# Optimization experiments

Hardware: AMD Instinct MI355X
Metric: run time of the kernel (lower is better)

The kernel has to match this reference:

```python
import jax, jax.numpy as jnp
import numpy as np

B, T, C, HS = 8, 2048, 1024, 64


def setup_inputs() -> dict:
    key = jax.random.key(0)
    kx, kq, kk, kv = jax.random.split(key, 4)
    x = jax.random.normal(kx, (B, T, C), dtype=jnp.float32)
    # torch Linear(C, HS, bias=False): weight [HS, C], y = x @ W.T -> store as [C, HS]
    Wq = jax.random.normal(kq, (C, HS), dtype=jnp.float32) * (C ** -0.5)
    Wk = jax.random.normal(kk, (C, HS), dtype=jnp.float32) * (C ** -0.5)
    Wv = jax.random.normal(kv, (C, HS), dtype=jnp.float32) * (C ** -0.5)
    return {"x": x, "Wq": Wq, "Wk": Wk, "Wv": Wv}


def reference(x, Wq, Wk, Wv):
    _, t, c = x.shape
    q = jnp.einsum('btc,ch->bth', x, Wq)
    k = jnp.einsum('btc,ch->bth', x, Wk)
    v = jnp.einsum('btc,ch->bth', x, Wv)
    # NOTE: original scales by C**-0.5 (hidden_dim), not head_size**-0.5
    scores = jnp.einsum('bth,bsh->bts', q, k) * (c ** -0.5)  # [B,T,T]
    causal = jnp.tril(jnp.ones((t, t), dtype=bool))
    scores = jnp.where(causal, scores, -jnp.inf)
    probs = jax.nn.softmax(scores, axis=-1)  # dropout p=0.0 -> identity
    out = jnp.einsum('bts,bsh->bth', probs, v)  # [B,T,HS]
    return out
```

## Files before the change

### kernel.cpp

```cpp
#include <hip/hip_runtime.h>
#include <hip/hip_bf16.h>

#define B_ 8
#define T_ 2048
#define C_ 1024
#define HS_ 64

typedef float f32x4 __attribute__((ext_vector_type(4)));
typedef __bf16 bf16x8 __attribute__((ext_vector_type(8)));
typedef __bf16 bf16x4 __attribute__((ext_vector_type(4)));

__device__ __forceinline__ void gld_lds16(const void* g, void* l) {
    __builtin_amdgcn_global_load_lds(
        (const __attribute__((address_space(1))) void*)g,
        (__attribute__((address_space(3))) void*)l, 16, 0, 0);
}


__global__ __launch_bounds__(256) void wt_kernel(const float* __restrict__ Wq,
                                                 const float* __restrict__ Wk,
                                                 const float* __restrict__ Wv,
                                                 __bf16* __restrict__ wt) {
    __shared__ float tile[64][65];
    int mb = blockIdx.x >> 4;
    int k0 = (blockIdx.x & 15) * 64;
    const float* W = (mb == 0) ? Wq : (mb == 1 ? Wk : Wv);
    int c = threadIdx.x & 63;
#pragma unroll
    for (int r = threadIdx.x >> 6; r < 64; r += 4)
        tile[r][c] = W[(size_t)(k0 + r) * 64 + c];
    __syncthreads();
    float scale = (mb == 0) ? 0.03125f : 1.0f;
    int kk = threadIdx.x & 63;
#pragma unroll
    for (int n = threadIdx.x >> 6; n < 64; n += 4) {
        int col = (((kk >> 3) ^ (n & 7)) * 8) + (kk & 7);
        wt[(size_t)(mb * 64 + n) * C_ + k0 + col] = (__bf16)(tile[kk][n] * scale);
    }
}

__global__ __launch_bounds__(512) void qkv_kernel(const float* __restrict__ x,
                                                  const __bf16* __restrict__ wt,
                                                  __bf16* __restrict__ qf,
                                                  __bf16* __restrict__ kf,
                                                  __bf16* __restrict__ vf) {
    __shared__ __align__(16) char smem[57344];
    __bf16* xs0 = (__bf16*)smem;
    __bf16* xs1 = (__bf16*)(smem + 4096);
    __bf16* ws0 = (__bf16*)(smem + 8192);
    __bf16* ws1 = (__bf16*)(smem + 32768);

    const int tid = threadIdx.x;
    const int w = tid >> 6, lane = tid & 63, lq = lane & 15, lg = lane >> 4;
    const int m0 = blockIdx.x * 32;
    const int mt = w & 1;
    const int ntb = (w >> 1) * 3;

    f32x4 acc[3];
#pragma unroll
    for (int i = 0; i < 3; ++i) acc[i] = (f32x4)0.0f;

    const int xrow = tid >> 3, xch = tid & 7;
    float4 xr0, xr1;
    const int wslot0 = w * 3 * 64 + lane;

    if (tid < 256) {
        const float* xp = x + (size_t)(m0 + xrow) * C_ + xch * 8;
        xr0 = *(const float4*)xp;
        xr1 = *(const float4*)(xp + 4);
    }
#pragma unroll
    for (int s = 0; s < 3; ++s) {
        int slot = wslot0 + s * 64;
        gld_lds16(wt + (size_t)(slot >> 3) * C_ + (slot & 7) * 8,
                  ws0 + (w * 3 + s) * 512);
    }
    if (tid < 256) {
        bf16x8 xb;
#pragma unroll
        for (int j = 0; j < 4; ++j) { xb[j] = (__bf16)xr0[j]; xb[4 + j] = (__bf16)xr1[j]; }
        *(bf16x8*)(xs0 + xrow * 64 + ((xch ^ (xrow & 7)) * 8)) = xb;
    }

    for (int kt = 0; kt < 16; ++kt) {
        __syncthreads();
        __bf16* xsc = (kt & 1) ? xs1 : xs0;
        __bf16* wsc = (kt & 1) ? ws1 : ws0;
        __bf16* xsn = (kt & 1) ? xs0 : xs1;
        __bf16* wsn = (kt & 1) ? ws0 : ws1;
        if (kt < 15) {
            int k0 = (kt + 1) * 64;
            if (tid < 256) {
                const float* xp = x + (size_t)(m0 + xrow) * C_ + k0 + xch * 8;
                xr0 = *(const float4*)xp;
                xr1 = *(const float4*)(xp + 4);
            }
#pragma unroll
            for (int s = 0; s < 3; ++s) {
                int slot = wslot0 + s * 64;
                gld_lds16(wt + (size_t)(slot >> 3) * C_ + k0 + (slot & 7) * 8,
                          wsn + (w * 3 + s) * 512);
            }
        }
#pragma unroll
        for (int ks = 0; ks < 2; ++ks) {
            int r = mt * 16 + lq;
            bf16x8 a = *(const bf16x8*)(xsc + r * 64 + (((ks * 4 + lg) ^ (r & 7)) * 8));
#pragma unroll
            for (int i = 0; i < 3; ++i) {
                int rw = (ntb + i) * 16 + lq;
                bf16x8 b = *(const bf16x8*)(wsc + rw * 64 + (((ks * 4 + lg) ^ (rw & 7)) * 8));
                acc[i] = __builtin_amdgcn_mfma_f32_16x16x32_bf16(a, b, acc[i], 0, 0, 0);
            }
        }
        if (kt < 15 && tid < 256) {
            bf16x8 xb;
#pragma unroll
            for (int j = 0; j < 4; ++j) { xb[j] = (__bf16)xr0[j]; xb[4 + j] = (__bf16)xr1[j]; }
            *(bf16x8*)(xsn + xrow * 64 + ((xch ^ (xrow & 7)) * 8)) = xb;
        }
    }
    __syncthreads();

    __bf16(*obuf)[208] = (__bf16(*)[208])smem;
#pragma unroll
    for (int i = 0; i < 3; ++i)
#pragma unroll
        for (int r = 0; r < 4; ++r)
            obuf[mt * 16 + lg * 4 + r][(ntb + i) * 16 + lq] = (__bf16)acc[i][r];
    __syncthreads();

    if (w < 4) {
        int mg = w & 1, half = w >> 1;
        size_t qt16 = (size_t)(m0 >> 4) + mg;
        bf16x8 vq = *(const bf16x8*)&obuf[mg * 16 + lq][half * 32 + lg * 8];
        bf16x8 vk = *(const bf16x8*)&obuf[mg * 16 + lq][64 + half * 32 + lg * 8];
        *(bf16x8*)(qf + ((qt16 * 2 + half) * 64 + lane) * 8) = vq;
        *(bf16x8*)(kf + ((qt16 * 2 + half) * 64 + lane) * 8) = vk;
    } else {
        int ntv = w - 4;
        bf16x8 vv;
#pragma unroll
        for (int j = 0; j < 8; ++j)
            vv[j] = obuf[lg * 8 + j][128 + ntv * 16 + lq];
        size_t kt32 = (size_t)(m0 >> 5);
        *(bf16x8*)(vf + ((kt32 * 4 + ntv) * 64 + lane) * 8) = vv;
    }
}

__global__ __launch_bounds__(512, 4) void attn_kernel(const __bf16* __restrict__ qf,
                                                      const __bf16* __restrict__ kf,
                                                      const __bf16* __restrict__ vf,
                                                      float* __restrict__ out) {
    __shared__ float olds[8][16][64];
    __shared__ float mlds[8][16], llds[8][16];
    __shared__ __align__(16) __bf16 plds[8][16 * 72];

    int w    = threadIdx.x >> 6;
    int lane = threadIdx.x & 63;
    int lq = lane & 15, lg = lane >> 4;

    int b  = blockIdx.x & 7;
    int q0 = (63 - (blockIdx.x >> 3)) * 32;
    int qs = w >> 2;
    int wk = w & 3;
    int qt = q0 + qs * 16;

    size_t qbase = ((size_t)b * 128 + (qt >> 4)) * 2;
    bf16x8 aq0 = *(const bf16x8*)(qf + ((qbase + 0) * 64 + lane) * 8);
    bf16x8 aq1 = *(const bf16x8*)(qf + ((qbase + 1) * 64 + lane) * 8);

    f32x4 o[4];
#pragma unroll
    for (int nt = 0; nt < 4; ++nt) o[nt] = (f32x4)0.0f;
    float m_s = -1e30f, l_s = 0.f;

    __bf16* pw = &plds[w][0];

    int ntiles = (qt + 79) >> 6;
    for (int kt = wk; kt < ntiles; kt += 4) {
        int s0 = kt * 64;
        f32x4 s[4];
        __builtin_amdgcn_s_setprio(1);
#pragma unroll
        for (int ct = 0; ct < 4; ++ct) {
            size_t kbase = ((size_t)b * 128 + (s0 >> 4) + ct) * 2;
            bf16x8 k0 = *(const bf16x8*)(kf + ((kbase + 0) * 64 + lane) * 8);
            bf16x8 k1 = *(const bf16x8*)(kf + ((kbase + 1) * 64 + lane) * 8);
            f32x4 a = (f32x4)0.0f;
            a = __builtin_amdgcn_mfma_f32_16x16x32_bf16(k0, aq0, a, 0, 0, 0);
            a = __builtin_amdgcn_mfma_f32_16x16x32_bf16(k1, aq1, a, 0, 0, 0);
            s[ct] = a;
        }
        __builtin_amdgcn_s_setprio(0);
        if (s0 + 63 > qt) {
#pragma unroll
            for (int ct = 0; ct < 4; ++ct)
#pragma unroll
                for (int r = 0; r < 4; ++r)
                    if (s0 + ct * 16 + lg * 4 + r > qt + lq) s[ct][r] = -1e30f;
        }
        bf16x8 bv[2][4];
#pragma unroll
        for (int ks = 0; ks < 2; ++ks)
#pragma unroll
            for (int nt = 0; nt < 4; ++nt)
                bv[ks][nt] = *(const bf16x8*)(vf +
                    (((size_t)(b * 64 + (s0 >> 5) + ks) * 4 + nt) * 64 + lane) * 8);
        float pm = -1e30f;
#pragma unroll
        for (int ct = 0; ct < 4; ++ct)
#pragma unroll
            for (int r = 0; r < 4; ++r) pm = fmaxf(pm, s[ct][r]);
        pm = fmaxf(pm, __shfl_xor(pm, 16));
        pm = fmaxf(pm, __shfl_xor(pm, 32));
        bool need = __any(pm > m_s);
        float al = 1.0f;
        if (need) {
            float mn = fmaxf(m_s, pm);
            al = __expf(m_s - mn);
            m_s = mn;
        }
        float rs = 0.f;
        f32x4 p[4];
#pragma unroll
        for (int ct = 0; ct < 4; ++ct)
#pragma unroll
            for (int r = 0; r < 4; ++r) {
                p[ct][r] = __expf(s[ct][r] - m_s);
                rs += p[ct][r];
            }
        rs += __shfl_xor(rs, 16);
        rs += __shfl_xor(rs, 32);
        if (need) {
            l_s = l_s * al + rs;
            float alr[4];
#pragma unroll
            for (int r = 0; r < 4; ++r) alr[r] = __shfl(al, lg * 4 + r);
#pragma unroll
            for (int nt = 0; nt < 4; ++nt)
#pragma unroll
                for (int r = 0; r < 4; ++r) o[nt][r] *= alr[r];
        } else {
            l_s += rs;
        }
#pragma unroll
        for (int ct = 0; ct < 4; ++ct) {
            bf16x4 qv;
#pragma unroll
            for (int r = 0; r < 4; ++r) qv[r] = (__bf16)p[ct][r];
            *(bf16x4*)&pw[lq * 72 + ct * 16 + lg * 4] = qv;
        }
        asm volatile("" ::: "memory");
        bf16x8 pa0 = *(const bf16x8*)&pw[lq * 72 + lg * 8];
        bf16x8 pa1 = *(const bf16x8*)&pw[lq * 72 + 32 + lg * 8];
        __builtin_amdgcn_s_setprio(1);
#pragma unroll
        for (int nt = 0; nt < 4; ++nt) {
            o[nt] = __builtin_amdgcn_mfma_f32_16x16x32_bf16(pa0, bv[0][nt], o[nt], 0, 0, 0);
            o[nt] = __builtin_amdgcn_mfma_f32_16x16x32_bf16(pa1, bv[1][nt], o[nt], 0, 0, 0);
        }
        __builtin_amdgcn_s_setprio(0);
    }

    asm volatile("" ::: "memory");
#pragma unroll
    for (int nt = 0; nt < 4; ++nt)
#pragma unroll
        for (int r = 0; r < 4; ++r)
            olds[w][lg * 4 + r][nt * 16 + lq] = o[nt][r];
    if (lg == 0) {
        mlds[w][lq] = m_s;
        llds[w][lq] = l_s;
    }
    __syncthreads();

    int row = threadIdx.x >> 4;
    int c4  = (threadIdx.x & 15) * 4;
    int wb  = (row >> 4) * 4;
    int r16 = row & 15;
    float M = -1e30f;
#pragma unroll
    for (int w2 = 0; w2 < 4; ++w2) M = fmaxf(M, mlds[wb + w2][r16]);
    float L = 0.f;
    f32x4 oa = (f32x4)0.0f;
#pragma unroll
    for (int w2 = 0; w2 < 4; ++w2) {
        float sc = __expf(mlds[wb + w2][r16] - M);
        L += sc * llds[wb + w2][r16];
        const float* op = &olds[wb + w2][r16][c4];
#pragma unroll
        for (int j = 0; j < 4; ++j) oa[j] += sc * op[j];
    }
    float inv = 1.0f / L;
    float4 st;
    st.x = oa[0] * inv; st.y = oa[1] * inv; st.z = oa[2] * inv; st.w = oa[3] * inv;
    *(float4*)(out + ((size_t)b * T_ + q0 + row) * HS_ + c4) = st;
}

extern "C" void kernel_launch(void* const* d_in, const int* in_sizes, int n_in,
                              void* d_out, int out_size, void* d_ws, size_t ws_size,
                              hipStream_t stream) {
    const float* x  = (const float*)d_in[0];
    const float* Wq = (const float*)d_in[1];
    const float* Wk = (const float*)d_in[2];
    const float* Wv = (const float*)d_in[3];
    char* ws = (char*)d_ws;
    __bf16* wt = (__bf16*)ws;
    __bf16* qf = (__bf16*)(ws + 393216);
    __bf16* kf = (__bf16*)(ws + 2490368);
    __bf16* vf = (__bf16*)(ws + 4587520);
    float* out = (float*)d_out;

    wt_kernel<<<dim3(48), dim3(256), 0, stream>>>(Wq, Wk, Wv, wt);
    qkv_kernel<<<dim3(512), dim3(512), 0, stream>>>(x, wt, qf, kf, vf);
    attn_kernel<<<dim3(512), dim3(512), 0, stream>>>(qf, kf, vf, out);
}
```

Baseline: 38.91 us.

## Halve attention key tile to 32 and alias LDS buffers for higher occupancy

Shrinks the per-iteration key tile from 64 to 32 columns, which cuts the score, P and V register footprint. Launch bounds rise to 8 blocks per CU. The P staging buffer and the final O reduction buffer now share one LDS allocation, separated by an extra barrier, to lower LDS per block. The aim is more resident waves to hide global-load latency, at the cost of twice as many loop iterations with more softmax and shuffle overhead per MFMA, and finer causal work balance.

New measurement: 53.84 us. 1.38x slower.

```diff
diff --git a/kernel.cpp b/kernel.cpp
--- a/kernel.cpp
+++ b/kernel.cpp
@@ -148,23 +148,22 @@
     }
 }
 
-__global__ __launch_bounds__(512, 4) void attn_kernel(const __bf16* __restrict__ qf,
+__global__ __launch_bounds__(512, 8) void attn_kernel(const __bf16* __restrict__ qf,
                                                       const __bf16* __restrict__ kf,
                                                       const __bf16* __restrict__ vf,
                                                       float* __restrict__ out) {
-    __shared__ float olds[8][16][64];
-    __shared__ float mlds[8][16], llds[8][16];
-    __shared__ __align__(16) __bf16 plds[8][16 * 72];
-
-    int w    = threadIdx.x >> 6;
-    int lane = threadIdx.x & 63;
-    int lq = lane & 15, lg = lane >> 4;
-
-    int b  = blockIdx.x & 7;
-    int q0 = (63 - (blockIdx.x >> 3)) * 32;
-    int qs = w >> 2;
-    int wk = w & 3;
-    int qt = q0 + qs * 16;
+    __shared__ __align__(16) char smem[33792];
+    float* mlds = (float*)(smem + 32768);
+    float* llds = (float*)(smem + 33280);
+
+    const int tid = threadIdx.x;
+    const int w = tid >> 6, lane = tid & 63, lq = lane & 15, lg = lane >> 4;
+
+    const int b  = blockIdx.x & 7;
+    const int q0 = (63 - (blockIdx.x >> 3)) * 32;
+    const int qs = w >> 2;
+    const int wk = w & 3;
+    const int qt = q0 + qs * 16;
 
     size_t qbase = ((size_t)b * 128 + (qt >> 4)) * 2;
     bf16x8 aq0 = *(const bf16x8*)(qf + ((qbase + 0) * 64 + lane) * 8);
@@ -175,15 +174,15 @@
     for (int nt = 0; nt < 4; ++nt) o[nt] = (f32x4)0.0f;
     float m_s = -1e30f, l_s = 0.f;
 
-    __bf16* pw = &plds[w][0];
-
-    int ntiles = (qt + 79) >> 6;
+    __bf16* pw = (__bf16*)(smem + w * 1280);
+
+    int ntiles = (qt + 47) >> 5;
     for (int kt = wk; kt < ntiles; kt += 4) {
-        int s0 = kt * 64;
-        f32x4 s[4];
+        int s0 = kt * 32;
+        f32x4 s[2];
         __builtin_amdgcn_s_setprio(1);
 #pragma unroll
-        for (int ct = 0; ct < 4; ++ct) {
+        for (int ct = 0; ct < 2; ++ct) {
             size_t kbase = ((size_t)b * 128 + (s0 >> 4) + ct) * 2;
             bf16x8 k0 = *(const bf16x8*)(kf + ((kbase + 0) * 64 + lane) * 8);
             bf16x8 k1 = *(const bf16x8*)(kf + ((kbase + 1) * 64 + lane) * 8);
@@ -193,25 +192,20 @@
             s[ct] = a;
         }
         __builtin_amdgcn_s_setprio(0);
-        if (s0 + 63 > qt) {
-#pragma unroll
-            for (int ct = 0; ct < 4; ++ct)
+        if (s0 + 31 > qt) {
+#pragma unroll
+            for (int ct = 0; ct < 2; ++ct)
 #pragma unroll
                 for (int r = 0; r < 4; ++r)
                     if (s0 + ct * 16 + lg * 4 + r > qt + lq) s[ct][r] = -1e30f;
         }
-        bf16x8 bv[2][4];
-#pragma unroll
-        for (int ks = 0; ks < 2; ++ks)
-#pragma unroll
-            for (int nt = 0; nt < 4; ++nt)
-                bv[ks][nt] = *(const bf16x8*)(vf +
-                    (((size_t)(b * 64 + (s0 >> 5) + ks) * 4 + nt) * 64 + lane) * 8);
-        float pm = -1e30f;
-#pragma unroll
-        for (int ct = 0; ct < 4; ++ct)
-#pragma unroll
-            for (int r = 0; r < 4; ++r) pm = fmaxf(pm, s[ct][r]);
+        bf16x8 bv[4];
+#pragma unroll
+        for (int nt = 0; nt < 4; ++nt)
+            bv[nt] = *(const bf16x8*)(vf +
+                (((size_t)(b * 64 + (s0 >> 5)) * 4 + nt) * 64 + lane) * 8);
+        float pm = fmaxf(fmaxf(fmaxf(s[0][0], s[0][1]), fmaxf(s[0][2], s[0][3])),
+                         fmaxf(fmaxf(s[1][0], s[1][1]), fmaxf(s[1][2], s[1][3])));
         pm = fmaxf(pm, __shfl_xor(pm, 16));
         pm = fmaxf(pm, __shfl_xor(pm, 32));
         bool need = __any(pm > m_s);
@@ -222,13 +216,12 @@
             m_s = mn;
         }
         float rs = 0.f;
-        f32x4 p[4];
-#pragma unroll
-        for (int ct = 0; ct < 4; ++ct)
+#pragma unroll
+        for (int ct = 0; ct < 2; ++ct)
 #pragma unroll
             for (int r = 0; r < 4; ++r) {
-                p[ct][r] = __expf(s[ct][r] - m_s);
-                rs += p[ct][r];
+                s[ct][r] = __expf(s[ct][r] - m_s);
+                rs += s[ct][r];
             }
         rs += __shfl_xor(rs, 16);
         rs += __shfl_xor(rs, 32);
@@ -245,50 +238,48 @@
             l_s += rs;
         }
 #pragma unroll
-        for (int ct = 0; ct < 4; ++ct) {
+        for (int ct = 0; ct < 2; ++ct) {
             bf16x4 qv;
 #pragma unroll
-            for (int r = 0; r < 4; ++r) qv[r] = (__bf16)p[ct][r];
-            *(bf16x4*)&pw[lq * 72 + ct * 16 + lg * 4] = qv;
+            for (int r = 0; r < 4; ++r) qv[r] = (__bf16)s[ct][r];
+            *(bf16x4*)&pw[lq * 40 + ct * 16 + lg * 4] = qv;
         }
         asm volatile("" ::: "memory");
-        bf16x8 pa0 = *(const bf16x8*)&pw[lq * 72 + lg * 8];
-        bf16x8 pa1 = *(const bf16x8*)&pw[lq * 72 + 32 + lg * 8];
+        bf16x8 pa = *(const bf16x8*)&pw[lq * 40 + lg * 8];
         __builtin_amdgcn_s_setprio(1);
 #pragma unroll
-        for (int nt = 0; nt < 4; ++nt) {
-            o[nt] = __builtin_amdgcn_mfma_f32_16x16x32_bf16(pa0, bv[0][nt], o[nt], 0, 0, 0);
-            o[nt] = __builtin_amdgcn_mfma_f32_16x16x32_bf16(pa1, bv[1][nt], o[nt], 0, 0, 0);
-        }
+        for (int nt = 0; nt < 4; ++nt)
+            o[nt] = __builtin_amdgcn_mfma_f32_16x16x32_bf16(pa, bv[nt], o[nt], 0, 0, 0);
         __builtin_amdgcn_s_setprio(0);
     }
 
-    asm volatile("" ::: "memory");
+    __syncthreads();
+    float* olds = (float*)smem;
 #pragma unroll
     for (int nt = 0; nt < 4; ++nt)
 #pragma unroll
         for (int r = 0; r < 4; ++r)
-            olds[w][lg * 4 + r][nt * 16 + lq] = o[nt][r];
+            olds[(w * 16 + lg * 4 + r) * 64 + nt * 16 + lq] = o[nt][r];
     if (lg == 0) {
-        mlds[w][lq] = m_s;
-        llds[w][lq] = l_s;
-    }
-    __syncthreads();
-
-    int row = threadIdx.x >> 4;
-    int c4  = (threadIdx.x & 15) * 4;
+        mlds[w * 16 + lq] = m_s;
+        llds[w * 16 + lq] = l_s;
+    }
+    __syncthreads();
+
+    int row = tid >> 4;
+    int c4  = (tid & 15) * 4;
     int wb  = (row >> 4) * 4;
     int r16 = row & 15;
     float M = -1e30f;
 #pragma unroll
-    for (int w2 = 0; w2 < 4; ++w2) M = fmaxf(M, mlds[wb + w2][r16]);
+    for (int w2 = 0; w2 < 4; ++w2) M = fmaxf(M, mlds[(wb + w2) * 16 + r16]);
     float L = 0.f;
     f32x4 oa = (f32x4)0.0f;
 #pragma unroll
     for (int w2 = 0; w2 < 4; ++w2) {
-        float sc = __expf(mlds[wb + w2][r16] - M);
-        L += sc * llds[wb + w2][r16];
-        const float* op = &olds[wb + w2][r16][c4];
+        float sc = __expf(mlds[(wb + w2) * 16 + r16] - M);
+        L += sc * llds[(wb + w2) * 16 + r16];
+        const float* op = olds + ((wb + w2) * 16 + r16) * 64 + c4;
 #pragma unroll
         for (int j = 0; j < 4; ++j) oa[j] += sc * op[j];
     }
```
